# Kernel tuning notes

Hardware: AMD Instinct MI355X
Metric: run time of the kernel (lower is better)

The kernel has to match this reference:

```python
import jax, jax.numpy as jnp
import numpy as np

NUM_EXPERTS = 64
TOPK = 8
NUM_TOKENS = 8192
HIDDEN = 4096


def setup_inputs() -> dict:
    key = jax.random.key(0)
    k1, k2 = jax.random.split(key)
    x = jax.random.normal(k1, (NUM_TOKENS, HIDDEN), dtype=jnp.float32)
    weight = jax.random.normal(k2, (NUM_EXPERTS, HIDDEN), dtype=jnp.float32) * 0.02
    return {"x": x, "weight": weight}


def reference(x, weight):
    # (1) router gating linear, performed in float32 (router_gating_linear)
    logits = jnp.einsum("th,eh->te", x.astype(jnp.float32), weight.astype(jnp.float32))
    # (2) score function: softmax over experts, then top-k selection
    scores = jax.nn.softmax(logits, axis=-1)  # [T, E]
    top_vals, top_idx = jax.lax.top_k(scores, TOPK)  # [T, K]
    rows = jnp.arange(scores.shape[0])[:, None]  # [T, 1]
    # probs: dense [T, E] with top-k weights scattered, zeros elsewhere
    probs = jnp.zeros_like(scores).at[rows, top_idx].set(top_vals)
    # routing_map: boolean token->expert assignment mask
    routing_map = jnp.zeros(scores.shape, dtype=bool).at[rows, top_idx].set(True)
    return probs, routing_map
```

## Files before the change

### kernel.cpp

```cpp
#include <hip/hip_runtime.h>

#define TOKENS 8192
#define EXPERTS 64
#define HIDDEN 4096
#define CHUNK 64
#define PAD 68

__global__ void transpose_w_kernel(const float* __restrict__ w,
                                   float* __restrict__ wT) {
    __shared__ float tile[64][65];
    const int tid = threadIdx.x;
    const int kb = blockIdx.x * 64;
#pragma unroll
    for (int p = 0; p < 16; ++p) {
        const int e = p * 4 + (tid >> 6);
        const int kk = tid & 63;
        tile[e][kk] = w[(size_t)e * HIDDEN + kb + kk];
    }
    __syncthreads();
#pragma unroll
    for (int q = 0; q < 16; ++q) {
        const int kr = q * 4 + (tid >> 6);
        const int ee = tid & 63;
        wT[(size_t)(kb + kr) * 64 + ee] = tile[ee][kr];
    }
}

__global__ __launch_bounds__(256, 6)
void logits_partial_kernel(const float* __restrict__ x,
                           const float* __restrict__ wT,
                           float* __restrict__ part,
                           int split, int kseg) {
    __shared__ float smem[64 * PAD];
    const int tid = threadIdx.x;
    const int lane = tid & 63;
    const int e0 = __builtin_amdgcn_readfirstlane((tid >> 6) * 16);
    const int g = blockIdx.x / split;
    const int s = blockIdx.x % split;
    const int t0 = g * 64;
    const int k0 = s * kseg;

    float acc[16];
#pragma unroll
    for (int j = 0; j < 16; ++j) acc[j] = 0.0f;

    const int rowb = tid >> 4;
    const int kk4 = (tid & 15) * 4;

    for (int c = 0; c < kseg; c += CHUNK) {
        __syncthreads();
#pragma unroll
        for (int p = 0; p < 4; ++p) {
            const int row = p * 16 + rowb;
            const float4 v = *reinterpret_cast<const float4*>(
                x + (size_t)(t0 + row) * HIDDEN + k0 + c + kk4);
            *reinterpret_cast<float4*>(&smem[row * PAD + kk4]) = v;
        }
        __syncthreads();

        const float* __restrict__ wbase = wT + (size_t)(k0 + c) * 64 + e0;
        for (int kk = 0; kk < CHUNK; kk += 4) {
            const float4 xv = *reinterpret_cast<const float4*>(
                &smem[lane * PAD + kk]);
            const float* __restrict__ wrow = wbase + (size_t)kk * 64;
#pragma unroll
            for (int j = 0; j < 16; ++j)
                acc[j] = fmaf(wrow[j], xv.x, acc[j]);
#pragma unroll
            for (int j = 0; j < 16; ++j)
                acc[j] = fmaf(wrow[64 + j], xv.y, acc[j]);
#pragma unroll
            for (int j = 0; j < 16; ++j)
                acc[j] = fmaf(wrow[128 + j], xv.z, acc[j]);
#pragma unroll
            for (int j = 0; j < 16; ++j)
                acc[j] = fmaf(wrow[192 + j], xv.w, acc[j]);
        }
    }

    float* dst = part + ((size_t)s * TOKENS + t0 + lane) * EXPERTS + e0;
#pragma unroll
    for (int j = 0; j < 16; j += 4) {
        float4 v = make_float4(acc[j], acc[j + 1], acc[j + 2], acc[j + 3]);
        *reinterpret_cast<float4*>(dst + j) = v;
    }
}

__global__ void reduce_topk_kernel(const float* __restrict__ part,
                                   float* __restrict__ out, int split) {
    const int wid = threadIdx.x >> 6;
    const int lane = threadIdx.x & 63;
    const int t = blockIdx.x * 4 + wid;

    float logit = 0.0f;
    for (int s = 0; s < split; ++s) {
        logit += part[((size_t)s * TOKENS + t) * EXPERTS + lane];
    }

    float m = logit;
#pragma unroll
    for (int off = 32; off >= 1; off >>= 1) m = fmaxf(m, __shfl_xor(m, off, 64));
    const float ex = __expf(logit - m);
    float sum = ex;
#pragma unroll
    for (int off = 32; off >= 1; off >>= 1) sum += __shfl_xor(sum, off, 64);
    const float score = ex / sum;

    float v = score;
    bool sel = false;
#pragma unroll
    for (int it = 0; it < 8; ++it) {
        float bv = v;
        int bi = lane;
#pragma unroll
        for (int off = 32; off >= 1; off >>= 1) {
            const float ov = __shfl_xor(bv, off, 64);
            const int oi = __shfl_xor(bi, off, 64);
            if (ov > bv || (ov == bv && oi < bi)) { bv = ov; bi = oi; }
        }
        if (lane == bi) { sel = true; v = -1.0f; }
    }

    out[(size_t)t * EXPERTS + lane] = sel ? score : 0.0f;
    out[(size_t)TOKENS * EXPERTS + (size_t)t * EXPERTS + lane] = sel ? 1.0f : 0.0f;
}

extern "C" void kernel_launch(void* const* d_in, const int* in_sizes, int n_in,
                              void* d_out, int out_size, void* d_ws, size_t ws_size,
                              hipStream_t stream) {
    (void)in_sizes; (void)n_in; (void)out_size;
    const float* x = (const float*)d_in[0];
    const float* w = (const float*)d_in[1];
    float* out = (float*)d_out;

    float* wT = (float*)d_ws;
    float* part = (float*)((char*)d_ws + (size_t)(1 << 20));

    int split = 16;
    while (split > 1 &&
           (size_t)(1 << 20) + (size_t)split * TOKENS * EXPERTS * 4 > ws_size) {
        split >>= 1;
    }
    const int kseg = HIDDEN / split;

    transpose_w_kernel<<<HIDDEN / 64, 256, 0, stream>>>(w, wT);
    logits_partial_kernel<<<(TOKENS / 64) * split, 256, 0, stream>>>(x, wT, part,
                                                                     split, kseg);
    reduce_topk_kernel<<<TOKENS / 4, 256, 0, stream>>>(part, out, split);
}
```

Before: 83.06 us.

## Double-buffer x tile via register prefetch and fix split at compile time

Prefetches the next x chunk into registers while the current chunk is computed from a double-buffered LDS tile, so global loads overlap the FMA loop. The split-K factor becomes a compile-time constant of 8 (was 16, or smaller if the workspace was short), which halves the partial-sum traffic and fully unrolls the reduce loop. Launch bounds drop to 4 waves per SIMD to make room for the extra registers and LDS. The change risks lower occupancy and fewer blocks, and it drops the workspace-size check.

```diff
diff --git a/kernel.cpp b/kernel.cpp
--- a/kernel.cpp
+++ b/kernel.cpp
@@ -3,7 +3,10 @@
 #define TOKENS 8192
 #define EXPERTS 64
 #define HIDDEN 4096
+#define SPLIT 8
+#define KSEG (HIDDEN / SPLIT)
 #define CHUNK 64
+#define NCH (KSEG / CHUNK)
 #define PAD 68
 
 __global__ void transpose_w_kernel(const float* __restrict__ w,
@@ -26,19 +29,18 @@
     }
 }
 
-__global__ __launch_bounds__(256, 6)
+__global__ __launch_bounds__(256, 4)
 void logits_partial_kernel(const float* __restrict__ x,
                            const float* __restrict__ wT,
-                           float* __restrict__ part,
-                           int split, int kseg) {
-    __shared__ float smem[64 * PAD];
+                           float* __restrict__ part) {
+    __shared__ float smem[2][64 * PAD];
     const int tid = threadIdx.x;
     const int lane = tid & 63;
     const int e0 = __builtin_amdgcn_readfirstlane((tid >> 6) * 16);
-    const int g = blockIdx.x / split;
-    const int s = blockIdx.x % split;
+    const int g = blockIdx.x / SPLIT;
+    const int s = blockIdx.x % SPLIT;
     const int t0 = g * 64;
-    const int k0 = s * kseg;
+    const int k0 = s * KSEG;
 
     float acc[16];
 #pragma unroll
@@ -46,22 +48,35 @@
 
     const int rowb = tid >> 4;
     const int kk4 = (tid & 15) * 4;
+    const float* __restrict__ xbase = x + (size_t)t0 * HIDDEN + k0;
 
-    for (int c = 0; c < kseg; c += CHUNK) {
-        __syncthreads();
+    float4 r[4];
+#pragma unroll
+    for (int p = 0; p < 4; ++p) {
+        r[p] = *reinterpret_cast<const float4*>(
+            xbase + (size_t)(p * 16 + rowb) * HIDDEN + kk4);
+    }
+
+    for (int c = 0; c < NCH; ++c) {
+        float* buf = smem[c & 1];
 #pragma unroll
         for (int p = 0; p < 4; ++p) {
-            const int row = p * 16 + rowb;
-            const float4 v = *reinterpret_cast<const float4*>(
-                x + (size_t)(t0 + row) * HIDDEN + k0 + c + kk4);
-            *reinterpret_cast<float4*>(&smem[row * PAD + kk4]) = v;
+            *reinterpret_cast<float4*>(&buf[(p * 16 + rowb) * PAD + kk4]) = r[p];
         }
         __syncthreads();
-
-        const float* __restrict__ wbase = wT + (size_t)(k0 + c) * 64 + e0;
+        if (c + 1 < NCH) {
+#pragma unroll
+            for (int p = 0; p < 4; ++p) {
+                r[p] = *reinterpret_cast<const float4*>(
+                    xbase + (size_t)(p * 16 + rowb) * HIDDEN
+                          + (c + 1) * CHUNK + kk4);
+            }
+        }
+        const float* __restrict__ wbase = wT + (size_t)(k0 + c * CHUNK) * 64 + e0;
+#pragma unroll 4
         for (int kk = 0; kk < CHUNK; kk += 4) {
             const float4 xv = *reinterpret_cast<const float4*>(
-                &smem[lane * PAD + kk]);
+                &buf[lane * PAD + kk]);
             const float* __restrict__ wrow = wbase + (size_t)kk * 64;
 #pragma unroll
             for (int j = 0; j < 16; ++j)
@@ -76,6 +91,7 @@
             for (int j = 0; j < 16; ++j)
                 acc[j] = fmaf(wrow[192 + j], xv.w, acc[j]);
         }
+        __syncthreads();
     }
 
     float* dst = part + ((size_t)s * TOKENS + t0 + lane) * EXPERTS + e0;
@@ -87,13 +103,14 @@
 }
 
 __global__ void reduce_topk_kernel(const float* __restrict__ part,
-                                   float* __restrict__ out, int split) {
+                                   float* __restrict__ out) {
     const int wid = threadIdx.x >> 6;
     const int lane = threadIdx.x & 63;
     const int t = blockIdx.x * 4 + wid;
 
     float logit = 0.0f;
-    for (int s = 0; s < split; ++s) {
+#pragma unroll
+    for (int s = 0; s < SPLIT; ++s) {
         logit += part[((size_t)s * TOKENS + t) * EXPERTS + lane];
     }
 
@@ -128,7 +145,7 @@
 extern "C" void kernel_launch(void* const* d_in, const int* in_sizes, int n_in,
                               void* d_out, int out_size, void* d_ws, size_t ws_size,
                               hipStream_t stream) {
-    (void)in_sizes; (void)n_in; (void)out_size;
+    (void)in_sizes; (void)n_in; (void)out_size; (void)ws_size;
     const float* x = (const float*)d_in[0];
     const float* w = (const float*)d_in[1];
     float* out = (float*)d_out;
@@ -136,15 +153,7 @@
     float* wT = (float*)d_ws;
     float* part = (float*)((char*)d_ws + (size_t)(1 << 20));
 
-    int split = 16;
-    while (split > 1 &&
-           (size_t)(1 << 20) + (size_t)split * TOKENS * EXPERTS * 4 > ws_size) {
-        split >>= 1;
-    }
-    const int kseg = HIDDEN / split;
-
     transpose_w_kernel<<<HIDDEN / 64, 256, 0, stream>>>(w, wT);
-    logits_partial_kernel<<<(TOKENS / 64) * split, 256, 0, stream>>>(x, wT, part,
-                                                                     split, kseg);
-    reduce_topk_kernel<<<TOKENS / 4, 256, 0, stream>>>(part, out, split);
+    logits_partial_kernel<<<(TOKENS / 64) * SPLIT, 256, 0, stream>>>(x, wT, part);
+    reduce_topk_kernel<<<TOKENS / 4, 256, 0, stream>>>(part, out);
 }
```

New measurement: 121.9 us. 46.7% more time.
